# Performance work log

Measured on AMD Instinct MI355X. Metric: run time of the kernel, lower is better.

Reference implementation:

```python
import jax, jax.numpy as jnp
import numpy as np

K = 15
P_DIM = 3
C_IN = 64
C_OUT = 64
KP_EXTENT = 0.06
RADIUS = 0.1
B, N, NNEIGHB = 1, 50000, 32


def _make_kernel_points(key):
    # Stand-in for load_kernels: K points in a sphere of given radius, first at center.
    pts = jax.random.normal(key, (K, P_DIM), dtype=jnp.float32)
    pts = pts / (jnp.linalg.norm(pts, axis=1, keepdims=True) + 1e-6)
    r = jax.random.uniform(jax.random.fold_in(key, 1), (K, 1), dtype=jnp.float32) ** (1.0 / P_DIM)
    pts = pts * r * RADIUS
    pts = pts.at[0].set(0.0)  # fixed 'center' point
    return pts


def setup_inputs() -> dict:
    key = jax.random.key(0)
    k1, k2, k3, k4, k5, k6, k7 = jax.random.split(key, 7)
    q_pts = jax.random.uniform(k1, (B, N, P_DIM), dtype=jnp.float32)
    s_pts = jax.random.uniform(k2, (B, 60000, P_DIM), dtype=jnp.float32)
    # neighbor coordinates near the query points (within conv radius)
    neighbors = q_pts[:, :, None, :] + (jax.random.uniform(k3, (B, N, NNEIGHB, P_DIM), dtype=jnp.float32) - 0.5) * (2 * RADIUS)
    neighb_inds = jax.random.randint(k4, (B, N, NNEIGHB), 0, 60000, dtype=jnp.int64)
    x = jax.random.normal(k5, (B, N, NNEIGHB, C_IN), dtype=jnp.float32)
    kernel_points = _make_kernel_points(k6)
    # kaiming_uniform_(a=sqrt(5)) on [K, C_in, C_out]: bound = sqrt(6/((1+5)*fan_in)), fan_in = C_in
    bound = float(np.sqrt(6.0 / (6.0 * C_IN)))
    weights = jax.random.uniform(k7, (K, C_IN, C_OUT), minval=-bound, maxval=bound, dtype=jnp.float32)
    return {"q_pts": q_pts, "s_pts": s_pts, "neighbors": neighbors,
            "neighb_inds": neighb_inds, "x": x,
            "kernel_points": kernel_points, "weights": weights}


def reference(q_pts, s_pts, neighbors, neighb_inds, x, kernel_points, weights):
    # Center neighbor coordinates on query points: [B,N,n,3]
    rel = neighbors - q_pts[:, :, None, :]
    # Differences to kernel points: [B,N,n,K,3]
    diff = rel[:, :, :, None, :] - kernel_points[None, None, None, :, :]
    sq_distances = jnp.sum(diff * diff, axis=-1)  # [B,N,n,K]
    # Linear influence, clamped at 0, transposed to [B,N,K,n]
    all_weights = jnp.clip(1.0 - jnp.sqrt(sq_distances) / KP_EXTENT, 0.0, None)
    all_weights = jnp.swapaxes(all_weights, -2, -1)
    # Weighted neighbor features per kernel point: [B,N,K,Cin]
    weighted = jnp.einsum('bnkm,bnmc->bnkc', all_weights, x)
    # Per-kernel-point matmul with weights [K,Cin,Cout], summed over K: [B,N,Cout]
    out = jnp.einsum('bnkc,kcd->bnd', weighted, weights)
    return out
```

## Files before the change

kernel.cpp:

```cpp
#include <hip/hip_runtime.h>


typedef __attribute__((ext_vector_type(8))) short bf16x8;
typedef __attribute__((ext_vector_type(4))) float f32x4;

#define NPTS        50000
#define PTS_PER_WG  16
#define KP_INV      (1.0f / 0.06f)

static __device__ __forceinline__ short f2bf(float f) {
    union { float f; unsigned u; } v; v.f = f;
    unsigned r = v.u + 0x7fffu + ((v.u >> 16) & 1u);
    return (short)(r >> 16);
}

__launch_bounds__(256, 4)
__global__ void kpconv_kernel(const float* __restrict__ q_pts,
                              const float* __restrict__ neighbors,
                              const float* __restrict__ x,
                              const float* __restrict__ kp,
                              const float* __restrict__ weights,
                              float* __restrict__ out) {
    __shared__ __align__(16) unsigned short wa[4][640];
    __shared__ __align__(16) unsigned short A2[PTS_PER_WG * 1024];

    const int tid   = threadIdx.x;
    const int wv    = tid >> 6;
    const int lane  = tid & 63;
    const int quad  = lane >> 4;
    const int r16   = lane & 15;
    const int wg    = blockIdx.x;

    const int m32   = lane & 31;
    const int khalf = lane >> 5;

    for (int i = 0; i < 4; ++i) {
        const int  p = wv * 4 + i;
        const long n = (long)wg * PTS_PER_WG + p;

        const float qx = q_pts[n*3 + 0];
        const float qy = q_pts[n*3 + 1];
        const float qz = q_pts[n*3 + 2];
        const float rx = neighbors[n*96 + m32*3 + 0] - qx;
        const float ry = neighbors[n*96 + m32*3 + 1] - qy;
        const float rz = neighbors[n*96 + m32*3 + 2] - qz;
        #pragma unroll
        for (int kk = 0; kk < 8; ++kk) {
            const int k  = kk * 2 + khalf;
            const int kc = (k < 15) ? k : 14;
            const float dx = rx - kp[kc*3 + 0];
            const float dy = ry - kp[kc*3 + 1];
            const float dz = rz - kp[kc*3 + 2];
            float w = 1.0f - sqrtf(dx*dx + dy*dy + dz*dz) * KP_INV;
            w = (k < 15) ? fmaxf(w, 0.0f) : 0.0f;
            wa[wv][k*40 + m32] = (unsigned short)f2bf(w);
        }
        __syncthreads();

        const bf16x8 af = *(const bf16x8*)&wa[wv][r16*40 + quad*8];

        const float* xp = x + n*2048 + (long)quad*512;
        #pragma unroll
        for (int t = 0; t < 4; ++t) {
            const int c = t*16 + r16;
            bf16x8 bf;
            #pragma unroll
            for (int j = 0; j < 8; ++j) bf[j] = f2bf(xp[c + j*64]);
            f32x4 acc = {0.f, 0.f, 0.f, 0.f};
            acc = __builtin_amdgcn_mfma_f32_16x16x32_bf16(af, bf, acc, 0, 0, 0);
            #pragma unroll
            for (int reg = 0; reg < 4; ++reg) {
                const int k  = quad*4 + reg;
                const int k2 = k*64 + c;
                const int ch = k2 >> 3;
                A2[p*1024 + ((ch ^ (p & 7)) << 3) + (k2 & 7)]
                    = (unsigned short)f2bf(acc[reg]);
            }
        }
    }

    __syncthreads();

    const int d = wv*16 + r16;
    f32x4 oacc = {0.f, 0.f, 0.f, 0.f};
    for (int kk = 0; kk < 30; ++kk) {
        const int ch = kk*4 + quad;
        const bf16x8 a2 = *(const bf16x8*)&A2[r16*1024 + ((ch ^ (r16 & 7)) << 3)];
        const float* wp = weights + (kk*32 + quad*8)*64 + d;
        bf16x8 bw;
        #pragma unroll
        for (int j = 0; j < 8; ++j) bw[j] = f2bf(wp[j*64]);
        oacc = __builtin_amdgcn_mfma_f32_16x16x32_bf16(a2, bw, oacc, 0, 0, 0);
    }

    #pragma unroll
    for (int reg = 0; reg < 4; ++reg) {
        const int p = quad*4 + reg;
        out[((long)wg * PTS_PER_WG + p)*64 + d] = oacc[reg];
    }
}

extern "C" void kernel_launch(void* const* d_in, const int* in_sizes, int n_in,
                              void* d_out, int out_size, void* d_ws, size_t ws_size,
                              hipStream_t stream) {
    const float* q_pts     = (const float*)d_in[0];
    const float* neighbors = (const float*)d_in[2];
    const float* x         = (const float*)d_in[4];
    const float* kp        = (const float*)d_in[5];
    const float* weights   = (const float*)d_in[6];
    float* out = (float*)d_out;

    dim3 grid(NPTS / PTS_PER_WG);
    kpconv_kernel<<<grid, 256, 0, stream>>>(q_pts, neighbors, x, kp, weights, out);
}
```

Baseline: 581.5 us.

## Compute kernel-point weights in registers and repack A2 layout to drop LDS barrier

Kernel-point influence weights are now computed directly in each lane's MFMA A-fragment registers from vectorized neighbor loads, removing the per-point shared staging buffer and its __syncthreads. bf16 conversion switches to a cheaper round-half-up pack via perm, and the intermediate A2 is stored as packed 2-element writes in a k-interleaved layout. The second GEMM then reads weights with a reordered K/C mapping over 32 iterations, using a dummy k index (zero A2 entries) for the 16th kernel point. Launch bounds are removed and the rounding mode changes slightly.

```diff
diff --git a/kernel.cpp b/kernel.cpp
--- a/kernel.cpp
+++ b/kernel.cpp
@@ -3,94 +3,107 @@
 
 typedef __attribute__((ext_vector_type(8))) short bf16x8;
 typedef __attribute__((ext_vector_type(4))) float f32x4;
+typedef __attribute__((ext_vector_type(4))) float floatx4;
+typedef __attribute__((ext_vector_type(2))) unsigned u32x2;
 
 #define NPTS        50000
 #define PTS_PER_WG  16
 #define KP_INV      (1.0f / 0.06f)
 
-static __device__ __forceinline__ short f2bf(float f) {
-    union { float f; unsigned u; } v; v.f = f;
-    unsigned r = v.u + 0x7fffu + ((v.u >> 16) & 1u);
-    return (short)(r >> 16);
+static __device__ __forceinline__ unsigned pack2bf(float lo, float hi) {
+    unsigned ul = __builtin_bit_cast(unsigned, lo) + 0x8000u;
+    unsigned uh = __builtin_bit_cast(unsigned, hi) + 0x8000u;
+    return __builtin_amdgcn_perm(uh, ul, 0x07060302u);
 }
 
-__launch_bounds__(256, 4)
 __global__ void kpconv_kernel(const float* __restrict__ q_pts,
                               const float* __restrict__ neighbors,
                               const float* __restrict__ x,
                               const float* __restrict__ kp,
                               const float* __restrict__ weights,
                               float* __restrict__ out) {
-    __shared__ __align__(16) unsigned short wa[4][640];
     __shared__ __align__(16) unsigned short A2[PTS_PER_WG * 1024];
 
-    const int tid   = threadIdx.x;
-    const int wv    = tid >> 6;
-    const int lane  = tid & 63;
-    const int quad  = lane >> 4;
-    const int r16   = lane & 15;
-    const int wg    = blockIdx.x;
+    const int tid  = threadIdx.x;
+    const int wv   = tid >> 6;
+    const int lane = tid & 63;
+    const int quad = lane >> 4;
+    const int r16  = lane & 15;
+    const int wg   = blockIdx.x;
 
-    const int m32   = lane & 31;
-    const int khalf = lane >> 5;
+    const int kr = (r16 < 15) ? r16 : 14;
+    const float kx = kp[kr*3 + 0], ky = kp[kr*3 + 1], kz = kp[kr*3 + 2];
 
+    #pragma unroll 1
     for (int i = 0; i < 4; ++i) {
-        const int  p = wv * 4 + i;
+        const int  p = wv*4 + i;
         const long n = (long)wg * PTS_PER_WG + p;
 
+        union { floatx4 v4[6]; float f[24]; } nb;
+        const floatx4* nptr = (const floatx4*)(neighbors + n*96 + quad*24);
+        #pragma unroll
+        for (int q2 = 0; q2 < 6; ++q2) nb.v4[q2] = nptr[q2];
         const float qx = q_pts[n*3 + 0];
         const float qy = q_pts[n*3 + 1];
         const float qz = q_pts[n*3 + 2];
-        const float rx = neighbors[n*96 + m32*3 + 0] - qx;
-        const float ry = neighbors[n*96 + m32*3 + 1] - qy;
-        const float rz = neighbors[n*96 + m32*3 + 2] - qz;
+
+        union { bf16x8 v; unsigned u[4]; } af;
         #pragma unroll
-        for (int kk = 0; kk < 8; ++kk) {
-            const int k  = kk * 2 + khalf;
-            const int kc = (k < 15) ? k : 14;
-            const float dx = rx - kp[kc*3 + 0];
-            const float dy = ry - kp[kc*3 + 1];
-            const float dz = rz - kp[kc*3 + 2];
-            float w = 1.0f - sqrtf(dx*dx + dy*dy + dz*dz) * KP_INV;
-            w = (k < 15) ? fmaxf(w, 0.0f) : 0.0f;
-            wa[wv][k*40 + m32] = (unsigned short)f2bf(w);
+        for (int jj = 0; jj < 4; ++jj) {
+            float w2[2];
+            #pragma unroll
+            for (int h = 0; h < 2; ++h) {
+                const int j = jj*2 + h;
+                const float dx = nb.f[3*j + 0] - qx - kx;
+                const float dy = nb.f[3*j + 1] - qy - ky;
+                const float dz = nb.f[3*j + 2] - qz - kz;
+                float w = 1.0f - sqrtf(dx*dx + dy*dy + dz*dz) * KP_INV;
+                w = fmaxf(w, 0.0f);
+                w2[h] = (r16 < 15) ? w : 0.0f;
+            }
+            af.u[jj] = pack2bf(w2[0], w2[1]);
         }
-        __syncthreads();
 
-        const bf16x8 af = *(const bf16x8*)&wa[wv][r16*40 + quad*8];
-
-        const float* xp = x + n*2048 + (long)quad*512;
+        const float* xp = x + n*2048 + quad*512;
+        const int sw = (p & 7) << 2;
         #pragma unroll
         for (int t = 0; t < 4; ++t) {
             const int c = t*16 + r16;
-            bf16x8 bf;
+            union { bf16x8 v; unsigned u[4]; } bf;
             #pragma unroll
-            for (int j = 0; j < 8; ++j) bf[j] = f2bf(xp[c + j*64]);
+            for (int jj = 0; jj < 4; ++jj)
+                bf.u[jj] = pack2bf(xp[(jj*2)*64 + c], xp[(jj*2 + 1)*64 + c]);
             f32x4 acc = {0.f, 0.f, 0.f, 0.f};
-            acc = __builtin_amdgcn_mfma_f32_16x16x32_bf16(af, bf, acc, 0, 0, 0);
-            #pragma unroll
-            for (int reg = 0; reg < 4; ++reg) {
-                const int k  = quad*4 + reg;
-                const int k2 = k*64 + c;
-                const int ch = k2 >> 3;
-                A2[p*1024 + ((ch ^ (p & 7)) << 3) + (k2 & 7)]
-                    = (unsigned short)f2bf(acc[reg]);
-            }
+            acc = __builtin_amdgcn_mfma_f32_16x16x32_bf16(af.v, bf.v, acc, 0, 0, 0);
+            const int Y = c*8 + quad*2;
+            u32x2 dd;
+            dd.x = pack2bf(acc[0], acc[1]);
+            dd.y = pack2bf(acc[2], acc[3]);
+            *(u32x2*)&A2[p*1024 + ((Y ^ sw) << 1)] = dd;
         }
     }
 
     __syncthreads();
 
-    const int d = wv*16 + r16;
+    const int d     = wv*16 + r16;
+    const int swr   = (r16 & 7) << 2;
+    const int kb    = (quad*8) & 15;
+    const int chalf = quad >> 1;
     f32x4 oacc = {0.f, 0.f, 0.f, 0.f};
-    for (int kk = 0; kk < 30; ++kk) {
-        const int ch = kk*4 + quad;
-        const bf16x8 a2 = *(const bf16x8*)&A2[r16*1024 + ((ch ^ (r16 & 7)) << 3)];
-        const float* wp = weights + (kk*32 + quad*8)*64 + d;
-        bf16x8 bw;
+    for (int kk = 0; kk < 32; ++kk) {
+        const int Y = kk*16 + quad*4;
+        const bf16x8 a2 = *(const bf16x8*)&A2[r16*1024 + ((Y ^ swr) << 1)];
+        const int c2 = kk*2 + chalf;
+        const float* wp = weights + c2*64 + d;
+        union { bf16x8 v; unsigned u[4]; } bw;
         #pragma unroll
-        for (int j = 0; j < 8; ++j) bw[j] = f2bf(wp[j*64]);
-        oacc = __builtin_amdgcn_mfma_f32_16x16x32_bf16(a2, bw, oacc, 0, 0, 0);
+        for (int jj = 0; jj < 4; ++jj) {
+            const int k0 = kb + jj*2;
+            int k1 = kb + jj*2 + 1;
+            if (k1 == 15) k1 = 0;
+            bw.u[jj] = pack2bf(wp[k0*4096], wp[k1*4096]);
+        }
+        oacc = __builtin_amdgcn_mfma_f32_16x16x32_bf16(a2, bw.v, oacc, 0, 0, 0);
     }
 
     #pragma unroll
```

Result: no change. 583.5 us (+0.3%).
